# Performance work log

Hardware: AMD Instinct MI355X
Metric: run time of the kernel (lower is better)

## Reference

```python
import jax, jax.numpy as jnp
import numpy as np

CUTOFF = 5.0
CUTOFF_ANGLE = 3.5
N = 25000
E = 800000
EA = 300000
T = 1600000
NBASIS = 8          # default radial basis size (bessel)
NBASIS_ANG = 8
DIM = 256
DIM_SRC = 64
DIM_DST = 32
DIM_ANGLE = 8
NMAX_ANGLE = 4
SPECIES_DIM = 16
NSPEC = 50


def bessel_basis(r, rc, n):
    # sin(k*pi*r/rc)/r Bessel-type radial basis, k=1..n  -> [E, n]
    x = r[:, None]
    k = jnp.arange(1, n + 1, dtype=r.dtype)[None, :] * (np.pi / rc)
    return jnp.sqrt(2.0 / rc) * jnp.sin(k * x) / x


def tssr2(x):
    # two-sided smooth square-root activation (identity inside |x|<=1)
    ax = jnp.abs(x)
    return jnp.where(ax <= 1.0, x, jnp.sign(x) * (2.0 * jnp.sqrt(jnp.maximum(ax, 1.0)) - 1.0))


def setup_inputs() -> dict:
    key = jax.random.key(0)
    ks = jax.random.split(key, 24)
    species = jax.random.randint(ks[0], (N,), 1, 17)
    edge_src = jax.random.randint(ks[1], (E,), 0, N)
    edge_dst = jax.random.randint(ks[2], (E,), 0, N)
    distances = 0.5 + jax.random.uniform(ks[3], (E,)) * (CUTOFF - 0.5)
    switch = 0.5 + 0.5 * jnp.cos(np.pi * distances / CUTOFF)
    angles = jax.random.uniform(ks[4], (T,)) * np.pi
    angle_src = jax.random.randint(ks[5], (T,), 0, EA)
    angle_dst = jax.random.randint(ks[6], (T,), 0, EA)
    central_atom = jax.random.randint(ks[7], (T,), 0, N)
    distances_angle = 0.5 + jax.random.uniform(ks[8], (EA,)) * (CUTOFF_ANGLE - 0.5)
    switch_angle = 0.5 + 0.5 * jnp.cos(np.pi * distances_angle / CUTOFF_ANGLE)
    s = lambda k, sh, scale: jax.random.normal(k, sh, jnp.float32) * scale
    din0 = SPECIES_DIM + DIM_SRC + NBASIS * DIM_DST + (NMAX_ANGLE + 1) * DIM_ANGLE  # 376
    din1 = DIM + DIM_SRC + NBASIS * DIM_DST + (NMAX_ANGLE + 1) * DIM_ANGLE          # 616
    return {
        'species': species, 'edge_src': edge_src, 'edge_dst': edge_dst,
        'distances': distances, 'switch': switch,
        'angles': angles, 'angle_src': angle_src, 'angle_dst': angle_dst,
        'central_atom': central_atom, 'distances_angle': distances_angle,
        'switch_angle': switch_angle,
        'species_table': s(ks[9], (NSPEC, SPECIES_DIM), 1.0),
        'W_si0': s(ks[10], (SPECIES_DIM, DIM_SRC + DIM_DST), SPECIES_DIM ** -0.5),
        'W_si1': s(ks[11], (DIM, DIM_SRC + DIM_DST), DIM ** -0.5),
        'W_da0': s(ks[12], (NBASIS_ANG, DIM_ANGLE), NBASIS_ANG ** -0.5),
        'W_da1': s(ks[13], (NBASIS_ANG, DIM_ANGLE), NBASIS_ANG ** -0.5),
        'W_mix0': s(ks[14], (din0, DIM), din0 ** -0.5),
        'b_mix0': jnp.zeros((DIM,), jnp.float32),
        'W_mix1': s(ks[15], (din1, DIM), din1 ** -0.5),
        'b_mix1': jnp.zeros((DIM,), jnp.float32),
    }


def reference(species, edge_src, edge_dst, distances, switch, angles, angle_src,
              angle_dst, central_atom, distances_angle, switch_angle,
              species_table, W_si0, W_si1, W_da0, W_da1,
              W_mix0, b_mix0, W_mix1, b_mix1):
    n_atoms = species.shape[0]
    # species encoding (learned/random table lookup)
    xi = species_table[species]                                   # [N, 16]
    # radial embeddings, smoothly switched at cutoff
    rb = bessel_basis(distances, CUTOFF, NBASIS) * switch[:, None]            # [E, 8]
    rba = bessel_basis(distances_angle, CUTOFF_ANGLE, NBASIS_ANG) * switch_angle[:, None]  # [EA, 8]
    # fourier angular features cos(n*theta), n=0..nmax_angle
    nvec = jnp.arange(NMAX_ANGLE + 1, dtype=angles.dtype)[None, :]
    xa = jnp.cos(nvec * angles[:, None])                          # [T, 5]
    for W_si, W_da, W_mix, b_mix in ((W_si0, W_da0, W_mix0, b_mix0),
                                     (W_si1, W_da1, W_mix1, b_mix1)):
        s = xi @ W_si                                             # [N, 96]
        si, si_dst = s[:, :DIM_SRC], s[:, DIM_SRC:]
        # radial message passing: outer(radial_basis, neighbor features) -> scatter-add
        mij = (rb[:, :, None] * si_dst[edge_dst][:, None, :]).reshape(rb.shape[0], -1)  # [E, 256]
        mi = jax.ops.segment_sum(mij, edge_src, num_segments=n_atoms)                   # [N, 256]
        # angular triplet features: pairwise vectors combined per angle
        da = rba @ W_da                                           # [EA, 8]
        dij = da[angle_src] * da[angle_dst]                       # [T, 8]
        ang = (xa[:, :, None] * dij[:, None, :]).reshape(xa.shape[0], -1)               # [T, 40]
        ami = jax.ops.segment_sum(ang, central_atom, num_segments=n_atoms)              # [N, 40]
        # mixing network + tssr2 mixing activation, residual when shapes match
        ei = jnp.concatenate([xi, si, mi, ami], axis=-1)
        dxi = tssr2(ei @ W_mix + b_mix)
        xi = xi + dxi if xi.shape[-1] == dxi.shape[-1] else dxi
    return xi
```

## Files before the change

### kernel.cpp

```cpp
#include <hip/hip_runtime.h>
#include <hip/hip_bf16.h>

typedef __hip_bfloat16 bf16;
typedef __bf16 bf8 __attribute__((ext_vector_type(8)));
typedef float  f4  __attribute__((ext_vector_type(4)));

#define N_ATOMS 25000
#define NE      800000
#define NEA     300000
#define NT      1600000
#define APB     64
#define NBUK    ((N_ATOMS + APB - 1) / APB)
#define PADB    512

#define DIN0  376
#define DIN1  616
#define DINP0 384
#define DINP1 640

#define EBLK ((NE + 4095) / 4096)
#define TBLK ((NT + 4095) / 4096)

#define NFRAG0 ((DINP0 / 32) * 16 * 64)
#define NFRAG1 ((DINP1 / 32) * 16 * 64)
#define NFRAGS (8 * 6 * 64)
#define WBLK   ((NFRAG0 + NFRAG1 + NFRAGS + 255) / 256)

#define S0BLK2 ((N_ATOMS * 120 + 511) / 512)
#define DABLK2 ((NEA + 1 + 511) / 512)

#define MIBLK ((N_ATOMS + 1) / 2)

__device__ __forceinline__ float tssr2f(float x) {
    float ax = fabsf(x);
    return (ax <= 1.f) ? x : copysignf(2.f * __builtin_sqrtf(ax) - 1.f, x);
}

__device__ __forceinline__ unsigned short f2bf_rn(float v) {
    unsigned int b = __float_as_uint(v);
    b += 0x7FFF + ((b >> 16) & 1);
    return (unsigned short)(b >> 16);
}
__device__ __forceinline__ float bf2f(unsigned short u) {
    return __uint_as_float(((unsigned int)u) << 16);
}

__device__ __forceinline__ void wprep_one(const float* __restrict__ W, bf8* __restrict__ Wf,
                                          int K, int N, int ntiles, int f) {
    int lane = f & 63;
    int ft = f >> 6;
    int tile = ft % ntiles;
    int chunk = ft / ntiles;
    int n = tile * 16 + (lane & 15);
    int kb = chunk * 32 + (lane >> 4) * 8;
    bf8 v;
#pragma unroll
    for (int j = 0; j < 8; j++) {
        int k = kb + j;
        v[j] = (__bf16)((k < K) ? W[k * N + n] : 0.f);
    }
    Wf[f] = v;
}

__global__ __launch_bounds__(256) void k_wc(const float* __restrict__ W0, bf8* __restrict__ Wf0,
                                            const float* __restrict__ W1, bf8* __restrict__ Wf1,
                                            const float* __restrict__ WS, bf8* __restrict__ WfS,
                                            const int* __restrict__ esrc, const int* __restrict__ cat,
                                            int* __restrict__ ebcnt, int* __restrict__ tbcnt) {
    int bid = blockIdx.x;
    int t = threadIdx.x;
    if (bid < WBLK) {
        int f = bid * 256 + t;
        if (f < NFRAG0) {
            wprep_one(W0, Wf0, DIN0, 256, 16, f);
        } else if (f < NFRAG0 + NFRAG1) {
            wprep_one(W1, Wf1, DIN1, 256, 16, f - NFRAG0);
        } else if (f < NFRAG0 + NFRAG1 + NFRAGS) {
            wprep_one(WS, WfS, 256, 96, 6, f - NFRAG0 - NFRAG1);
        }
        return;
    }
    bid -= WBLK;
    __shared__ int h[NBUK];
    for (int b = t; b < NBUK; b += 256) h[b] = 0;
    __syncthreads();
    bool isE = bid < EBLK;
    const int* key = isE ? esrc : cat;
    int n = isE ? NE : NT;
    int base = (isE ? bid : bid - EBLK) * 4096;
#pragma unroll
    for (int k = 0; k < 16; k++) {
        int idx = base + k * 256 + t;
        if (idx < n) atomicAdd(&h[key[idx] >> 6], 1);
    }
    __syncthreads();
    int* g = isE ? ebcnt : tbcnt;
    for (int b = t; b < NBUK; b += 256)
        if (h[b]) atomicAdd(&g[b], h[b]);
}

__global__ __launch_bounds__(512) void k_scanB(const int* cnt0, int* off0, int* cur0,
                                               const int* cnt1, int* off1, int* cur1) {
    const int* cnt = blockIdx.x ? cnt1 : cnt0;
    int* off = blockIdx.x ? off1 : off0;
    int* cur = blockIdx.x ? cur1 : cur0;
    __shared__ int sh[512];
    int t = threadIdx.x;
    int v = (t < NBUK) ? cnt[t] : 0;
    sh[t] = v;
    __syncthreads();
    for (int d = 1; d < 512; d <<= 1) {
        int a = (t >= d) ? sh[t - d] : 0;
        __syncthreads();
        sh[t] += a;
        __syncthreads();
    }
    int excl = sh[t] - v;
    if (t <= NBUK) { off[t] = excl; if (t < NBUK) cur[t] = excl; }
}

__global__ __launch_bounds__(512) void k_bpre(const float* __restrict__ eA,
                                              const float* __restrict__ eB,
                                              const int* __restrict__ eC,
                                              const int* __restrict__ ekey,
                                              int* __restrict__ egcur,
                                              float4* __restrict__ ebuk,
                                              const float* __restrict__ tA,
                                              const int* __restrict__ tB,
                                              const int* __restrict__ tC,
                                              const int* __restrict__ tkey,
                                              int* __restrict__ tgcur,
                                              float4* __restrict__ tbuk,
                                              const int* __restrict__ sp,
                                              const float* __restrict__ table,
                                              const float* __restrict__ Wsi,
                                              unsigned short* __restrict__ ei0,
                                              float* __restrict__ sd,
                                              const float* __restrict__ dist,
                                              const float* __restrict__ sw2,
                                              const float* __restrict__ Wda0,
                                              const float* __restrict__ Wda1,
                                              unsigned short* __restrict__ dah0,
                                              unsigned short* __restrict__ dah1) {
    int bid = blockIdx.x;
    int t = threadIdx.x;
    if (bid < EBLK + TBLK) {
        __shared__ int cnt[NBUK];
        __shared__ int rbase[NBUK];
        for (int b = t; b < NBUK; b += 512) cnt[b] = 0;
        __syncthreads();
        bool isE = bid < EBLK;
        const int* key = isE ? ekey : tkey;
        int n = isE ? NE : NT;
        int* gcur = isE ? egcur : tgcur;
        float4* buk = isE ? ebuk : tbuk;
        int base = (isE ? bid : (bid - EBLK)) * 4096;
        float4 pay[8];
        int bk[8], off[8];
#pragma unroll
        for (int k = 0; k < 8; k++) {
            int idx = base + k * 512 + t;
            bk[k] = -1;
            if (idx < n) {
                float4 p;
                if (isE) {
                    p.x = eA[idx];
                    p.y = eB[idx];
                    p.z = __int_as_float(eC[idx]);
                } else {
                    p.x = __cosf(tA[idx]);
                    p.y = __int_as_float(tB[idx]);
                    p.z = __int_as_float(tC[idx]);
                }
                int ky = key[idx];
                p.w = __int_as_float(ky);
                pay[k] = p;
                bk[k] = ky >> 6;
                off[k] = atomicAdd(&cnt[bk[k]], 1);
            }
        }
        __syncthreads();
        for (int b = t; b < NBUK; b += 512)
            if (cnt[b]) rbase[b] = atomicAdd(&gcur[b], cnt[b]);
        __syncthreads();
#pragma unroll
        for (int k = 0; k < 8; k++)
            if (bk[k] >= 0) buk[rbase[bk[k]] + off[k]] = pay[k];
    } else if (bid < EBLK + TBLK + S0BLK2) {
        int idx = (bid - EBLK - TBLK) * 512 + t;
        if (idx >= N_ATOMS * 120) return;
        int i = idx / 120;
        int c = idx - i * 120;
        if (c >= 112) {
            ei0[(size_t)i * DINP0 + 376 + (c - 112)] = 0;
            return;
        }
        int s = sp[i];
        if (c < 16) {
            ei0[(size_t)i * DINP0 + c] = f2bf_rn(table[s * 16 + c]);
        } else {
            int cc = c - 16;
            float acc = 0.f;
#pragma unroll
            for (int k = 0; k < 16; k++)
                acc += table[s * 16 + k] * Wsi[k * 96 + cc];
            if (cc < 64) ei0[(size_t)i * DINP0 + 16 + cc] = f2bf_rn(acc);
            else         sd[i * 32 + cc - 64]             = acc;
        }
    } else {
        int e = (bid - EBLK - TBLK - S0BLK2) * 512 + t;
        if (e > NEA) return;
        if (e == NEA) {
            uint4 z = make_uint4(0, 0, 0, 0);
            *(uint4*)&dah0[(size_t)e * 8] = z;
            *(uint4*)&dah1[(size_t)e * 8] = z;
            return;
        }
        float d = dist[e];
        float s = sw2[e];
        float rb[8];
#pragma unroll
        for (int n = 0; n < 8; n++)
            rb[n] = 0.7559289460f * __sinf((n + 1) * 0.8975979010f * d) / d * s;
        unsigned short h0[8], h1[8];
#pragma unroll
        for (int c = 0; c < 8; c++) {
            float a0 = 0.f, a1 = 0.f;
#pragma unroll
            for (int n = 0; n < 8; n++) {
                a0 += rb[n] * Wda0[n * 8 + c];
                a1 += rb[n] * Wda1[n * 8 + c];
            }
            h0[c] = f2bf_rn(a0);
            h1[c] = f2bf_rn(a1);
        }
        *(uint4*)&dah0[e * 8] = *(uint4*)h0;
        *(uint4*)&dah1[e * 8] = *(uint4*)h1;
    }
}

__global__ __launch_bounds__(256) void k_binB2(const int* __restrict__ ebkoff,
                                               const int* __restrict__ ebcnt,
                                               const float4* __restrict__ ebuk,
                                               float* __restrict__ erb,
                                               int* __restrict__ edi,
                                               int* __restrict__ ebase_g,
                                               int* __restrict__ epcnt_g,
                                               const int* __restrict__ tbkoff,
                                               const int* __restrict__ tbcnt,
                                               const float4* __restrict__ tbuk,
                                               float4* __restrict__ tpay,
                                               int* __restrict__ tbase_g,
                                               int* __restrict__ tpcnt_g) {
    bool isE = blockIdx.x < NBUK;
    int b = isE ? blockIdx.x : (blockIdx.x - NBUK);
    const int* bkoff = isE ? ebkoff : tbkoff;
    const int* bkcnt = isE ? ebcnt : tbcnt;
    const float4* buk = isE ? ebuk : tbuk;
    int* baseg = isE ? ebase_g : tbase_g;
    int* pcntg = isE ? epcnt_g : tpcnt_g;
    int lo = b * APB;
    int hi = min(lo + APB, N_ATOMS);
    int sbase = bkoff[b];
    int bc = bkcnt[b];
    int fb = sbase + b * PADB;
    __shared__ int cntA[APB];
    __shared__ int abase[APB];
    __shared__ int cur[APB];
    int t = threadIdx.x;
    if (t < APB) cntA[t] = 0;
    __syncthreads();
    for (int p = sbase + t; p < sbase + bc; p += 256) {
        int a = __float_as_int(((const float*)(buk + p))[3]);
        atomicAdd(&cntA[a - lo], 1);
    }
    __syncthreads();
    if (t == 0) {
        int run = fb;
        for (int k = 0; k < hi - lo; k++) {
            int pc = (cntA[k] + 7) & ~7;
            abase[k] = run;
            cur[k] = run;
            baseg[lo + k] = run;
            pcntg[lo + k] = pc;
            run += pc;
        }
    }
    __syncthreads();
    if (t < hi - lo) {
        int c = cntA[t];
        int pc = (c + 7) & ~7;
        int base = abase[t];
        if (isE) {
            for (int s = base + c; s < base + pc; s++) {
                edi[s] = 0;
                int pos = s - base;
                float* dz = erb + ((size_t)base + (pos & ~7)) * 8 + (pos & 7);
#pragma unroll
                for (int nn = 0; nn < 8; nn++) dz[nn * 8] = 0.f;
            }
        } else {
            float4 pz = make_float4(0.f, __int_as_float(NEA), __int_as_float(NEA), 0.f);
            for (int s = base + c; s < base + pc; s++) tpay[s] = pz;
        }
    }
    __syncthreads();
    for (int p = sbase + t; p < sbase + bc; p += 256) {
        float4 pay = buk[p];
        int a = __float_as_int(pay.w);
        int k = a - lo;
        int slot = atomicAdd(&cur[k], 1);
        if (isE) {
            float d = pay.x, s2 = pay.y;
            float q = 0.6324555320f * s2 / d;
            int pos = slot - abase[k];
            float* dst = erb + ((size_t)abase[k] + (pos & ~7)) * 8 + (pos & 7);
#pragma unroll
            for (int nn = 0; nn < 8; nn++)
                dst[nn * 8] = q * __sinf((nn + 1) * 0.6283185307f * d);
            edi[slot] = __float_as_int(pay.z);
        } else {
            tpay[slot] = pay;
        }
    }
}

__global__ __launch_bounds__(256) void k_s1(const unsigned short* __restrict__ ei1,
                                            const bf8* __restrict__ Wf,
                                            unsigned short* __restrict__ ei1o,
                                            float* __restrict__ sd) {
    __shared__ __align__(16) __bf16 Asg[4][64][8];
    int t = threadIdx.x;
    int w = t >> 6, lane = t & 63;
    int a0 = blockIdx.x * 64;

    int satom = a0 + (t >> 2);
    int k8 = (t & 3) * 8;
    const unsigned short* arow = &ei1[(size_t)satom * DINP1 + k8];
    bool aok = satom < N_ATOMS;
    int dw = (t >> 2) >> 4;
    int dl = ((t >> 2) & 15) | ((t & 3) << 4);
    __bf16* adst = &Asg[dw][dl][0];

    f4 acc[6];
#pragma unroll
    for (int j = 0; j < 6; j++) {
        f4 z = {0.f, 0.f, 0.f, 0.f};
        acc[j] = z;
    }

    for (int ch = 0; ch < 8; ch++) {
        uint4 v = make_uint4(0, 0, 0, 0);
        if (aok) v = *(const uint4*)(arow + ch * 32);
        __syncthreads();
        *(uint4*)adst = v;
        __syncthreads();
        bf8 afr = *(const bf8*)&Asg[w][lane][0];
        const bf8* wp = &Wf[(ch * 6) * 64 + lane];
#pragma unroll
        for (int tn = 0; tn < 6; tn++) {
            bf8 b = wp[tn * 64];
            acc[tn] = __builtin_amdgcn_mfma_f32_16x16x32_bf16(afr, b, acc[tn], 0, 0, 0);
        }
    }

    int nlo = lane & 15, q = lane >> 4;
#pragma unroll
    for (int r = 0; r < 4; r++) {
        int atom = a0 + w * 16 + q * 4 + r;
        if (atom < N_ATOMS) {
#pragma unroll
            for (int tn = 0; tn < 6; tn++) {
                int col = tn * 16 + nlo;
                float v = acc[tn][r];
                if (col < 64) ei1o[(size_t)atom * DINP1 + 256 + col] = f2bf_rn(v);
                else          sd[atom * 32 + col - 64] = v;
            }
        }
    }
    for (int z = t; z < 64 * 24; z += 256) {
        int za = a0 + z / 24;
        if (za < N_ATOMS) ei1o[(size_t)za * DINP1 + 616 + z % 24] = 0;
    }
}

__device__ __forceinline__ void ami_win(const float4 twA, const unsigned short* __restrict__ dah,
                                        int gmax, int jj, int c,
                                        float& a0, float& a1, float& a2, float& a3, float& a4) {
    float sc = 0.f; unsigned short dA = 0, dB = 0;
    {
        sc = __shfl(twA.x, jj, 64);
        int ea = __float_as_int(__shfl(twA.y, jj, 64));
        int eb = __float_as_int(__shfl(twA.z, jj, 64));
        dA = dah[ea * 8 + c];
        dB = dah[eb * 8 + c];
    }
    for (int g = 0; g < gmax; g++) {
        float scN = 0.f; unsigned short dAN = 0, dBN = 0;
        if (g + 1 < gmax) {
            int sl = (g + 1) * 8 + jj;
            scN = __shfl(twA.x, sl, 64);
            int ea = __float_as_int(__shfl(twA.y, sl, 64));
            int eb = __float_as_int(__shfl(twA.z, sl, 64));
            dAN = dah[ea * 8 + c];
            dBN = dah[eb * 8 + c];
        }
        float dij = bf2f(dA) * bf2f(dB);
        float c1 = sc;
        float c2 = __builtin_fmaf(2.f * c1, c1, -1.f);
        float c3 = __builtin_fmaf(2.f * c1, c2, -c1);
        float c4 = __builtin_fmaf(2.f * c1, c3, -c2);
        a0 += dij;
        a1 = __builtin_fmaf(c1, dij, a1);
        a2 = __builtin_fmaf(c2, dij, a2);
        a3 = __builtin_fmaf(c3, dij, a3);
        a4 = __builtin_fmaf(c4, dij, a4);
        if (g + 1 < gmax) { sc = scN; dA = dAN; dB = dBN; }
    }
}

__global__ __launch_bounds__(256) void k_seg(const int* __restrict__ ebase,
                                             const int* __restrict__ epcnt,
                                             const float* __restrict__ erb,
                                             const int* __restrict__ edi,
                                             const float* __restrict__ sd,
                                             unsigned short* __restrict__ mo, int mstride,
                                             const int* __restrict__ tbase,
                                             const int* __restrict__ tpcnt,
                                             const float4* __restrict__ tpay,
                                             const unsigned short* __restrict__ dah,
                                             unsigned short* __restrict__ ao, int astride) {
    __shared__ float4 smi[2][64];
    __shared__ float  sam[2][5][8];
    int t = threadIdx.x;
    int wv = t >> 6, l = t & 63;
    int slot = wv >> 1;
    int p    = wv & 1;

    if ((int)blockIdx.x < MIBLK) {
        int i = blockIdx.x * 2 + slot;
        bool valid = (i < N_ATOMS);
        int pbeg = 0, pcnt = 0;
        if (valid) { pbeg = tbase[i]; pcnt = tpcnt[i]; }
        int jj = l >> 3, c = l & 7;
        float a0 = 0.f, a1 = 0.f, a2 = 0.f, a3 = 0.f, a4 = 0.f;

        if (pcnt > 0) {
            int nG = pcnt >> 3;
            if (pcnt <= 128) {
                int h0 = (nG + 1) >> 1;
                int gb = p ? h0 : 0;
                int myg = p ? (nG - h0) : h0;
                if (myg > 0) {
                    int tb = gb * 8;
                    float4 twA = tpay[pbeg + tb + min(l, myg * 8 - 1)];
                    ami_win(twA, dah, myg, jj, c, a0, a1, a2, a3, a4);
                }
            } else {
                int nW = (pcnt + 63) >> 6;
                for (int W = p; W < nW; W += 2) {
                    int wbase = W * 64;
                    int rem = pcnt - wbase;
                    int lim = min(rem, 64);
                    float4 twA = tpay[pbeg + wbase + min(l, rem - 1)];
                    ami_win(twA, dah, lim >> 3, jj, c, a0, a1, a2, a3, a4);
                }
            }
        }

#pragma unroll
        for (int msk = 8; msk <= 32; msk <<= 1) {
            a0 += __shfl_xor(a0, msk, 64);
            a1 += __shfl_xor(a1, msk, 64);
            a2 += __shfl_xor(a2, msk, 64);
            a3 += __shfl_xor(a3, msk, 64);
            a4 += __shfl_xor(a4, msk, 64);
        }
        if (p == 1 && l < 8) {
            sam[slot][0][l] = a0; sam[slot][1][l] = a1; sam[slot][2][l] = a2;
            sam[slot][3][l] = a3; sam[slot][4][l] = a4;
        }
        __syncthreads();
        if (valid && p == 0 && l < 8) {
            a0 += sam[slot][0][l]; a1 += sam[slot][1][l]; a2 += sam[slot][2][l];
            a3 += sam[slot][3][l]; a4 += sam[slot][4][l];
            unsigned short* o = &ao[(size_t)i * astride + c];
            o[0]  = f2bf_rn(a0);
            o[8]  = f2bf_rn(a1);
            o[16] = f2bf_rn(a2);
            o[24] = f2bf_rn(a3);
            o[32] = f2bf_rn(a4);
        }
    } else {
        int i = ((int)blockIdx.x - MIBLK) * 2 + slot;
        bool valid = (i < N_ATOMS);
        int pbeg = 0, pcnt = 0;
        if (valid) { pbeg = ebase[i]; pcnt = epcnt[i]; }
        int n = l >> 3, cb = (l & 7) * 4;
        float4 acc = make_float4(0.f, 0.f, 0.f, 0.f);

        if (pcnt > 0) {
            int nG = pcnt >> 3;
            int h0 = (nG + 1) >> 1;
            int gbeg = p ? h0 : 0;
            int gend = p ? nG : h0;
            if (pcnt <= 64) {
                int eWin = edi[pbeg + min(l, pcnt - 1)];
                for (int g = gbeg; g < gend; g++) {
                    const float* rp = erb + ((size_t)pbeg + g * 8) * 8 + n * 8;
                    f4 rA = *(const f4*)rp;
                    f4 rB = *(const f4*)(rp + 4);
                    float4 v[8];
#pragma unroll
                    for (int j = 0; j < 8; j++) {
                        int eid = __shfl(eWin, g * 8 + j, 64);
                        v[j] = *(const float4*)&sd[eid * 32 + cb];
                    }
#pragma unroll
                    for (int j = 0; j < 8; j++) {
                        float rbj = (j < 4) ? rA[j] : rB[j - 4];
                        acc.x += rbj * v[j].x; acc.y += rbj * v[j].y;
                        acc.z += rbj * v[j].z; acc.w += rbj * v[j].w;
                    }
                }
            } else {
                const int* dp = edi + pbeg;
                for (int g = gbeg; g < gend; g++) {
                    const float* rp = erb + ((size_t)pbeg + g * 8) * 8 + n * 8;
                    f4 rA = *(const f4*)rp;
                    f4 rB = *(const f4*)(rp + 4);
                    float4 v[8];
#pragma unroll
                    for (int j = 0; j < 8; j++) {
                        int eid = dp[g * 8 + j];
                        v[j] = *(const float4*)&sd[eid * 32 + cb];
                    }
#pragma unroll
                    for (int j = 0; j < 8; j++) {
                        float rbj = (j < 4) ? rA[j] : rB[j - 4];
                        acc.x += rbj * v[j].x; acc.y += rbj * v[j].y;
                        acc.z += rbj * v[j].z; acc.w += rbj * v[j].w;
                    }
                }
            }
        }

        if (p == 1) smi[slot][l] = acc;
        __syncthreads();
        if (valid && p == 0) {
            float4 o = smi[slot][l];
            acc.x += o.x; acc.y += o.y; acc.z += o.z; acc.w += o.w;
            ushort4 pk = make_ushort4(f2bf_rn(acc.x), f2bf_rn(acc.y),
                                      f2bf_rn(acc.z), f2bf_rn(acc.w));
            *(ushort4*)&mo[(size_t)i * mstride + l * 4] = pk;
        }
    }
}

template <int LAYER>
__global__ __launch_bounds__(256) void k_gemm(const unsigned short* __restrict__ ei,
                                              const bf8* __restrict__ Wf,
                                              const float* __restrict__ bias,
                                              const unsigned short* __restrict__ skip,
                                              float* __restrict__ outf,
                                              unsigned short* __restrict__ outb) {
    constexpr int DINP = (LAYER == 0) ? DINP0 : DINP1;
    constexpr int NCH = DINP / 32;
    __shared__ __align__(16) __bf16 Asg[2][64][8];
    int t = threadIdx.x;
    int w = t >> 6, lane = t & 63;
    int a0 = blockIdx.x * 32;

    int f  = t * 4;
    int tA = f >> 9;
    int al = (f >> 3) & 63;
    int j0 = f & 7;
    int sm = al & 15, sq = al >> 4;
    int ga = a0 + tA * 16 + sm;
    const unsigned short* arow = &ei[(size_t)ga * DINP + sq * 8 + j0];
    __bf16* adst = &Asg[0][0][0] + f;
    bool aok = (ga < N_ATOMS);

    f4 acc[2][4];
#pragma unroll
    for (int i = 0; i < 2; i++)
#pragma unroll
        for (int j = 0; j < 4; j++) {
            f4 z = {0.f, 0.f, 0.f, 0.f};
            acc[i][j] = z;
        }

    for (int ch = 0; ch < NCH; ch++) {
        uint2 v = make_uint2(0, 0);
        if (aok) v = *(const uint2*)(arow + ch * 32);
        __syncthreads();
        *(uint2*)adst = v;
        __syncthreads();
        bf8 afr0 = *(const bf8*)&Asg[0][lane][0];
        bf8 afr1 = *(const bf8*)&Asg[1][lane][0];
        const bf8* wp = &Wf[(ch * 16 + w * 4) * 64 + lane];
#pragma unroll
        for (int tn = 0; tn < 4; tn++) {
            bf8 b = wp[tn * 64];
            acc[0][tn] = __builtin_amdgcn_mfma_f32_16x16x32_bf16(afr0, b, acc[0][tn], 0, 0, 0);
            acc[1][tn] = __builtin_amdgcn_mfma_f32_16x16x32_bf16(afr1, b, acc[1][tn], 0, 0, 0);
        }
    }

    int nlo = lane & 15, q = lane >> 4;
#pragma unroll
    for (int tA2 = 0; tA2 < 2; tA2++) {
#pragma unroll
        for (int r = 0; r < 4; r++) {
            int atom = a0 + tA2 * 16 + q * 4 + r;
            if (atom < N_ATOMS) {
#pragma unroll
                for (int tn = 0; tn < 4; tn++) {
                    int col = w * 64 + tn * 16 + nlo;
                    float vv = tssr2f(acc[tA2][tn][r] + bias[col]);
                    if (LAYER == 0) {
                        outb[(size_t)atom * DINP1 + col] = f2bf_rn(vv);
                    } else {
                        outf[(size_t)atom * 256 + col] =
                            vv + bf2f(skip[(size_t)atom * DINP1 + col]);
                    }
                }
            }
        }
    }
}

extern "C" void kernel_launch(void* const* d_in, const int* in_sizes, int n_in,
                              void* d_out, int out_size, void* d_ws, size_t ws_size,
                              hipStream_t stream) {
    const int*   species     = (const int*)d_in[0];
    const int*   edge_src    = (const int*)d_in[1];
    const int*   edge_dst    = (const int*)d_in[2];
    const float* distances   = (const float*)d_in[3];
    const float* sw          = (const float*)d_in[4];
    const float* angles      = (const float*)d_in[5];
    const int*   angle_src   = (const int*)d_in[6];
    const int*   angle_dst   = (const int*)d_in[7];
    const int*   central     = (const int*)d_in[8];
    const float* dist_a      = (const float*)d_in[9];
    const float* sw_a        = (const float*)d_in[10];
    const float* table       = (const float*)d_in[11];
    const float* W_si0       = (const float*)d_in[12];
    const float* W_si1       = (const float*)d_in[13];
    const float* W_da0       = (const float*)d_in[14];
    const float* W_da1       = (const float*)d_in[15];
    const float* W_mix0      = (const float*)d_in[16];
    const float* b_mix0      = (const float*)d_in[17];
    const float* W_mix1      = (const float*)d_in[18];
    const float* b_mix1      = (const float*)d_in[19];
    float* out = (float*)d_out;

    char* p = (char*)d_ws;
    auto alloc = [&](size_t bytes) {
        char* r = p;
        p += (bytes + 255) & ~(size_t)255;
        return (void*)r;
    };
    unsigned short* ei0 = (unsigned short*)alloc((size_t)N_ATOMS * DINP0 * 2);
    unsigned short* ei1 = (unsigned short*)alloc((size_t)N_ATOMS * DINP1 * 2);
    float*  sd   = (float*)alloc((size_t)N_ATOMS * 32 * 4);
    unsigned short* dah0 = (unsigned short*)alloc((size_t)(NEA + 1) * 8 * 2);
    unsigned short* dah1 = (unsigned short*)alloc((size_t)(NEA + 1) * 8 * 2);
    float*  erbf = (float*)alloc((size_t)(NE + NBUK * PADB) * 8 * 4);
    int*    edi  = (int*)alloc((size_t)(NE + NBUK * PADB) * 4);
    float4* tpay = (float4*)alloc((size_t)(NT + NBUK * PADB) * 16);
    float4* ebuk = (float4*)alloc((size_t)NE * 16);
    bf8*    Wf0  = (bf8*)alloc((size_t)NFRAG0 * 16);
    bf8*    Wf1  = (bf8*)alloc((size_t)NFRAG1 * 16);
    bf8*    WfS1 = (bf8*)alloc((size_t)NFRAGS * 16);
    int* ebase  = (int*)alloc((size_t)N_ATOMS * 4);
    int* epcnt  = (int*)alloc((size_t)N_ATOMS * 4);
    int* tbase  = (int*)alloc((size_t)N_ATOMS * 4);
    int* tpcnt  = (int*)alloc((size_t)N_ATOMS * 4);
    int* bcnt   = (int*)alloc((size_t)2 * NBUK * 4);
    int* ebkoff = (int*)alloc((size_t)(NBUK + 1) * 4);
    int* tbkoff = (int*)alloc((size_t)(NBUK + 1) * 4);
    int* gce    = (int*)alloc((size_t)NBUK * 4);
    int* gct    = (int*)alloc((size_t)NBUK * 4);
    (void)ws_size;
    int* ebcnt = bcnt;
    int* tbcnt = bcnt + NBUK;

    float4* tbuk = (float4*)ei1;

    hipMemsetAsync(bcnt, 0, (size_t)2 * NBUK * 4, stream);

    k_wc<<<WBLK + EBLK + TBLK, 256, 0, stream>>>(
        W_mix0, Wf0, W_mix1, Wf1, W_si1, WfS1,
        edge_src, central, ebcnt, tbcnt);

    k_scanB<<<2, 512, 0, stream>>>(ebcnt, ebkoff, gce, tbcnt, tbkoff, gct);

    k_bpre<<<EBLK + TBLK + S0BLK2 + DABLK2, 512, 0, stream>>>(
        distances, sw, edge_dst, edge_src, gce, ebuk,
        angles, angle_src, angle_dst, central, gct, tbuk,
        species, table, W_si0, ei0, sd,
        dist_a, sw_a, W_da0, W_da1, dah0, dah1);

    k_binB2<<<2 * NBUK, 256, 0, stream>>>(
        ebkoff, ebcnt, ebuk, erbf, edi, ebase, epcnt,
        tbkoff, tbcnt, tbuk, tpay, tbase, tpcnt);

    int gemm_grid = (N_ATOMS + 31) / 32;

    k_seg<<<2 * MIBLK, 256, 0, stream>>>(ebase, epcnt, erbf, edi, sd, ei0 + 80, DINP0,
                                         tbase, tpcnt, tpay, dah0, ei0 + 336, DINP0);
    k_gemm<0><<<gemm_grid, 256, 0, stream>>>(ei0, Wf0, b_mix0, nullptr, nullptr, ei1);

    k_s1<<<(N_ATOMS + 63) / 64, 256, 0, stream>>>(ei1, WfS1, ei1, sd);
    k_seg<<<2 * MIBLK, 256, 0, stream>>>(ebase, epcnt, erbf, edi, sd, ei1 + 320, DINP1,
                                         tbase, tpcnt, tpay, dah1, ei1 + 576, DINP1);
    k_gemm<1><<<gemm_grid, 256, 0, stream>>>(ei1, Wf1, b_mix1, ei1, out, nullptr);
}
```

Before: 413.0 us.

## Store radial basis edge-major and broadcast via shuffles; batch angular gathers

```diff
diff --git a/kernel.cpp b/kernel.cpp
--- a/kernel.cpp
+++ b/kernel.cpp
@@ -292,12 +292,11 @@
         int pc = (c + 7) & ~7;
         int base = abase[t];
         if (isE) {
+            float4 z = make_float4(0.f, 0.f, 0.f, 0.f);
             for (int s = base + c; s < base + pc; s++) {
                 edi[s] = 0;
-                int pos = s - base;
-                float* dz = erb + ((size_t)base + (pos & ~7)) * 8 + (pos & 7);
-#pragma unroll
-                for (int nn = 0; nn < 8; nn++) dz[nn * 8] = 0.f;
+                *(float4*)&erb[(size_t)s * 8]     = z;
+                *(float4*)&erb[(size_t)s * 8 + 4] = z;
             }
         } else {
             float4 pz = make_float4(0.f, __int_as_float(NEA), __int_as_float(NEA), 0.f);
@@ -313,11 +312,12 @@
         if (isE) {
             float d = pay.x, s2 = pay.y;
             float q = 0.6324555320f * s2 / d;
-            int pos = slot - abase[k];
-            float* dst = erb + ((size_t)abase[k] + (pos & ~7)) * 8 + (pos & 7);
+            float r[8];
 #pragma unroll
             for (int nn = 0; nn < 8; nn++)
-                dst[nn * 8] = q * __sinf((nn + 1) * 0.6283185307f * d);
+                r[nn] = q * __sinf((nn + 1) * 0.6283185307f * d);
+            *(float4*)&erb[(size_t)slot * 8]     = make_float4(r[0], r[1], r[2], r[3]);
+            *(float4*)&erb[(size_t)slot * 8 + 4] = make_float4(r[4], r[5], r[6], r[7]);
             edi[slot] = __float_as_int(pay.z);
         } else {
             tpay[slot] = pay;
@@ -387,35 +387,33 @@
 __device__ __forceinline__ void ami_win(const float4 twA, const unsigned short* __restrict__ dah,
                                         int gmax, int jj, int c,
                                         float& a0, float& a1, float& a2, float& a3, float& a4) {
-    float sc = 0.f; unsigned short dA = 0, dB = 0;
-    {
-        sc = __shfl(twA.x, jj, 64);
-        int ea = __float_as_int(__shfl(twA.y, jj, 64));
-        int eb = __float_as_int(__shfl(twA.z, jj, 64));
-        dA = dah[ea * 8 + c];
-        dB = dah[eb * 8 + c];
-    }
-    for (int g = 0; g < gmax; g++) {
-        float scN = 0.f; unsigned short dAN = 0, dBN = 0;
-        if (g + 1 < gmax) {
-            int sl = (g + 1) * 8 + jj;
-            scN = __shfl(twA.x, sl, 64);
+    float scv[8];
+    unsigned short dAv[8], dBv[8];
+#pragma unroll
+    for (int g = 0; g < 8; g++) {
+        if (g < gmax) {
+            int sl = g * 8 + jj;
+            scv[g] = __shfl(twA.x, sl, 64);
             int ea = __float_as_int(__shfl(twA.y, sl, 64));
             int eb = __float_as_int(__shfl(twA.z, sl, 64));
-            dAN = dah[ea * 8 + c];
-            dBN = dah[eb * 8 + c];
-        }
-        float dij = bf2f(dA) * bf2f(dB);
-        float c1 = sc;
-        float c2 = __builtin_fmaf(2.f * c1, c1, -1.f);
-        float c3 = __builtin_fmaf(2.f * c1, c2, -c1);
-        float c4 = __builtin_fmaf(2.f * c1, c3, -c2);
-        a0 += dij;
-        a1 = __builtin_fmaf(c1, dij, a1);
-        a2 = __builtin_fmaf(c2, dij, a2);
-        a3 = __builtin_fmaf(c3, dij, a3);
-        a4 = __builtin_fmaf(c4, dij, a4);
-        if (g + 1 < gmax) { sc = scN; dA = dAN; dB = dBN; }
+            dAv[g] = dah[ea * 8 + c];
+            dBv[g] = dah[eb * 8 + c];
+        }
+    }
+#pragma unroll
+    for (int g = 0; g < 8; g++) {
+        if (g < gmax) {
+            float dij = bf2f(dAv[g]) * bf2f(dBv[g]);
+            float c1 = scv[g];
+            float c2 = __builtin_fmaf(2.f * c1, c1, -1.f);
+            float c3 = __builtin_fmaf(2.f * c1, c2, -c1);
+            float c4 = __builtin_fmaf(2.f * c1, c3, -c2);
+            a0 += dij;
+            a1 = __builtin_fmaf(c1, dij, a1);
+            a2 = __builtin_fmaf(c2, dij, a2);
+            a3 = __builtin_fmaf(c3, dij, a3);
+            a4 = __builtin_fmaf(c4, dij, a4);
+        }
     }
 }
 
@@ -506,29 +504,30 @@
             int gend = p ? nG : h0;
             if (pcnt <= 64) {
                 int eWin = edi[pbeg + min(l, pcnt - 1)];
-                for (int g = gbeg; g < gend; g++) {
-                    const float* rp = erb + ((size_t)pbeg + g * 8) * 8 + n * 8;
-                    f4 rA = *(const f4*)rp;
-                    f4 rB = *(const f4*)(rp + 4);
-                    float4 v[8];
-#pragma unroll
-                    for (int j = 0; j < 8; j++) {
-                        int eid = __shfl(eWin, g * 8 + j, 64);
-                        v[j] = *(const float4*)&sd[eid * 32 + cb];
-                    }
-#pragma unroll
-                    for (int j = 0; j < 8; j++) {
-                        float rbj = (j < 4) ? rA[j] : rB[j - 4];
-                        acc.x += rbj * v[j].x; acc.y += rbj * v[j].y;
-                        acc.z += rbj * v[j].z; acc.w += rbj * v[j].w;
+                if (gbeg < gend) {
+                    float cA = erb[((size_t)pbeg + gbeg * 8) * 8 + l];
+                    for (int g = gbeg; g < gend; g++) {
+                        float4 v[8];
+#pragma unroll
+                        for (int j = 0; j < 8; j++) {
+                            int eid = __shfl(eWin, g * 8 + j, 64);
+                            v[j] = *(const float4*)&sd[eid * 32 + cb];
+                        }
+                        float cB = 0.f;
+                        if (g + 1 < gend) cB = erb[((size_t)pbeg + g * 8 + 8) * 8 + l];
+#pragma unroll
+                        for (int j = 0; j < 8; j++) {
+                            float rbj = __shfl(cA, j * 8 + n, 64);
+                            acc.x += rbj * v[j].x; acc.y += rbj * v[j].y;
+                            acc.z += rbj * v[j].z; acc.w += rbj * v[j].w;
+                        }
+                        if (g + 1 < gend) cA = cB;
                     }
                 }
             } else {
                 const int* dp = edi + pbeg;
                 for (int g = gbeg; g < gend; g++) {
-                    const float* rp = erb + ((size_t)pbeg + g * 8) * 8 + n * 8;
-                    f4 rA = *(const f4*)rp;
-                    f4 rB = *(const f4*)(rp + 4);
+                    const float* rp = erb + ((size_t)pbeg + g * 8) * 8 + n;
                     float4 v[8];
 #pragma unroll
                     for (int j = 0; j < 8; j++) {
@@ -537,7 +536,7 @@
                     }
 #pragma unroll
                     for (int j = 0; j < 8; j++) {
-                        float rbj = (j < 4) ? rA[j] : rB[j - 4];
+                        float rbj = rp[j * 8];
                         acc.x += rbj * v[j].x; acc.y += rbj * v[j].y;
                         acc.z += rbj * v[j].z; acc.w += rbj * v[j].w;
                     }
```

New measurement: 401.0 us. 1.03x faster.
